# Kernel optimization log

Hardware: AMD Instinct MI355X
Metric: run time of the kernel (lower is better)

## Reference

```python
import jax, jax.numpy as jnp
import numpy as np

N_EXPERTS = 64
TOP_K = 2
LOAD_BALANCE_COEF = 0.01
D_MODEL = 4096
N_TOKENS = 16384


def setup_inputs() -> dict:
    key = jax.random.key(0)
    kx, kw = jax.random.split(key)
    x = jax.random.normal(kx, (N_TOKENS, D_MODEL), dtype=jnp.float32)
    # nn.init.normal_(gate.weight, std=0.01); shape (n_experts, d_model)
    gate_w = 0.01 * jax.random.normal(kw, (N_EXPERTS, D_MODEL), dtype=jnp.float32)
    return {"x": x, "gate_w": gate_w}


def reference(x, gate_w):
    # logits: (N, n_experts)
    logits = jnp.einsum('nd,ed->ne', x, gate_w)
    router_probs = jax.nn.softmax(logits, axis=-1)
    top_k_weights, top_k_indices = jax.lax.top_k(router_probs, TOP_K)
    routing_weights = top_k_weights / jnp.sum(top_k_weights, axis=-1, keepdims=True)
    top1 = top_k_indices[:, 0]
    one_hot = jax.nn.one_hot(top1, N_EXPERTS, dtype=x.dtype)  # (N, n_experts)
    f_i = jnp.mean(one_hot, axis=0)          # fraction of tokens per expert (detached)
    p_i = jnp.mean(router_probs, axis=0)     # mean router prob per expert (diff.)
    load_balance_loss = LOAD_BALANCE_COEF * jnp.sum(jax.lax.stop_gradient(f_i) * p_i)
    return routing_weights, top_k_indices, load_balance_loss
```

## Files before the change

kernel.cpp:

```cpp
#include <hip/hip_runtime.h>
#include <math.h>

#define N_TOKENS 16384
#define D_MODEL  4096
#define N_EXP    64

#define BK   16
#define LD   68
#define KW   (D_MODEL / 4)
#define NT   (KW / BK)
#define NBLK (N_TOKENS / 64)

__global__ void __launch_bounds__(256)
router_fused(const float* __restrict__ x, const float* __restrict__ w,
             float* __restrict__ out, float* __restrict__ block_sums) {
    __shared__ float smem[4 * 4 * BK * LD + 2 * 4 * N_EXP];

    const int tid  = threadIdx.x;
    const int wv   = tid >> 6;
    const int lane = tid & 63;
    const int tok0 = blockIdx.x * 64;

    float* xs  = smem + wv * (4 * BK * LD);
    float* wsb = xs + 2 * BK * LD;

    const int srow = lane >> 2;
    const int skc  = (lane & 3) * 4;

    const int tg   = lane & 7;
    const int eg   = lane >> 3;
    const int trow = tg * 8;
    const int ecol = eg * 8;

    const float* xp = x + (size_t)(tok0 + srow) * D_MODEL + (size_t)wv * KW + skc;
    const float* wp = w + (size_t)srow * D_MODEL + (size_t)wv * KW + skc;

    float acc[8][8] = {};

#define LOADR(q, roff) (*(const float4*)((q) + (size_t)(roff) * D_MODEL))
#define STORE_TILE(buf, v, roff) do {                      \
        (buf)[(skc + 0) * LD + srow + (roff)] = (v).x;     \
        (buf)[(skc + 1) * LD + srow + (roff)] = (v).y;     \
        (buf)[(skc + 2) * LD + srow + (roff)] = (v).z;     \
        (buf)[(skc + 3) * LD + srow + (roff)] = (v).w;     \
    } while (0)

    {
        float4 a0 = LOADR(xp, 0),  a1 = LOADR(xp, 16);
        float4 a2 = LOADR(xp, 32), a3 = LOADR(xp, 48);
        float4 b0 = LOADR(wp, 0),  b1 = LOADR(wp, 16);
        float4 b2 = LOADR(wp, 32), b3 = LOADR(wp, 48);
        STORE_TILE(xs, a0, 0);  STORE_TILE(xs, a1, 16);
        STORE_TILE(xs, a2, 32); STORE_TILE(xs, a3, 48);
        STORE_TILE(wsb, b0, 0);  STORE_TILE(wsb, b1, 16);
        STORE_TILE(wsb, b2, 32); STORE_TILE(wsb, b3, 48);
    }

    auto compute_tile = [&](const float* xb, const float* wb) {
#pragma unroll
        for (int k = 0; k < BK; ++k) {
            const float* xr = xb + k * LD + trow;
            const float* wr = wb + k * LD + ecol;
            float4 xa = *(const float4*)xr;
            float4 xc = *(const float4*)(xr + 4);
            float4 wa = *(const float4*)wr;
            float4 wc = *(const float4*)(wr + 4);
            float xf[8] = {xa.x, xa.y, xa.z, xa.w, xc.x, xc.y, xc.z, xc.w};
            float wf[8] = {wa.x, wa.y, wa.z, wa.w, wc.x, wc.y, wc.z, wc.w};
#pragma unroll
            for (int i = 0; i < 8; ++i)
#pragma unroll
                for (int j = 0; j < 8; ++j)
                    acc[i][j] = fmaf(xf[i], wf[j], acc[i][j]);
        }
    };

#pragma unroll 2
    for (int t = 0; t < NT - 1; ++t) {
        float* xb = xs  + (t & 1) * (BK * LD);
        float* wb = wsb + (t & 1) * (BK * LD);
        float* xn = xs  + ((t + 1) & 1) * (BK * LD);
        float* wn = wsb + ((t + 1) & 1) * (BK * LD);

        const float* xq = xp + (t + 1) * BK;
        const float* wq = wp + (t + 1) * BK;
        float4 a0 = LOADR(xq, 0),  a1 = LOADR(xq, 16);
        float4 a2 = LOADR(xq, 32), a3 = LOADR(xq, 48);
        float4 b0 = LOADR(wq, 0),  b1 = LOADR(wq, 16);
        float4 b2 = LOADR(wq, 32), b3 = LOADR(wq, 48);

        compute_tile(xb, wb);

        STORE_TILE(xn, a0, 0);  STORE_TILE(xn, a1, 16);
        STORE_TILE(xn, a2, 32); STORE_TILE(xn, a3, 48);
        STORE_TILE(wn, b0, 0);  STORE_TILE(wn, b1, 16);
        STORE_TILE(wn, b2, 32); STORE_TILE(wn, b3, 48);
    }
    compute_tile(xs + ((NT - 1) & 1) * (BK * LD), wsb + ((NT - 1) & 1) * (BK * LD));

    __syncthreads();

    float* tile = smem + wv * 4096;
#pragma unroll
    for (int i = 0; i < 8; ++i) {
        *(float4*)&tile[(trow + i) * 64 + ecol] =
            make_float4(acc[i][0], acc[i][1], acc[i][2], acc[i][3]);
        *(float4*)&tile[(trow + i) * 64 + ecol + 4] =
            make_float4(acc[i][4], acc[i][5], acc[i][6], acc[i][7]);
    }
    __syncthreads();

    float p_acc = 0.f, f_acc = 0.f;
#pragma unroll 1
    for (int it = 0; it < 16; ++it) {
        const int tl = wv * 16 + it;
        const int o  = tl * 64 + lane;
        float logit = smem[o] + smem[4096 + o] + smem[8192 + o] + smem[12288 + o];

        float m = logit;
#pragma unroll
        for (int off = 32; off; off >>= 1)
            m = fmaxf(m, __shfl_xor(m, off, 64));
        unsigned long long b1 = __ballot(logit == m);
        int i1 = __ffsll(b1) - 1;

        float p = expf(logit - m);
        float denom = p;
#pragma unroll
        for (int off = 32; off; off >>= 1)
            denom += __shfl_xor(denom, off, 64);

        p_acc += p / denom;
        if (lane == i1) f_acc += 1.f;

        float lx = (lane == i1) ? -__builtin_inff() : logit;
        float m2 = lx;
#pragma unroll
        for (int off = 32; off; off >>= 1)
            m2 = fmaxf(m2, __shfl_xor(m2, off, 64));
        unsigned long long b2 = __ballot(lx == m2);
        int i2 = __ffsll(b2) - 1;

        if (lane == 0) {
            float p1 = 1.0f / denom;
            float p2 = expf(m2 - m) / denom;
            float s12 = p1 + p2;
            int token = tok0 + tl;
            ((float2*)out)[token] = make_float2(p1 / s12, p2 / s12);
            ((float2*)(out + 2 * N_TOKENS))[token] =
                make_float2((float)i1, (float)i2);
        }
    }

    float* pf = smem + 4 * 4 * BK * LD;
    pf[wv * 64 + lane]       = p_acc;
    pf[256 + wv * 64 + lane] = f_acc;
    __syncthreads();
    if (tid < N_EXP) {
        float ps = pf[tid] + pf[64 + tid] + pf[128 + tid] + pf[192 + tid];
        float fs = pf[256 + tid] + pf[320 + tid] + pf[384 + tid] + pf[448 + tid];
        block_sums[(size_t)blockIdx.x * 128 + tid]      = ps;
        block_sums[(size_t)blockIdx.x * 128 + 64 + tid] = fs;
    }
}

__global__ void __launch_bounds__(256)
router_final(const float* __restrict__ block_sums, float* __restrict__ out) {
    __shared__ float sp[4][N_EXP];
    __shared__ float sf[4][N_EXP];

    int tid  = threadIdx.x;
    int wv   = tid >> 6;
    int lane = tid & 63;

    float ps = 0.f, fs = 0.f;
#pragma unroll 8
    for (int b = wv * (NBLK / 4); b < (wv + 1) * (NBLK / 4); ++b) {
        ps += block_sums[(size_t)b * 128 + lane];
        fs += block_sums[(size_t)b * 128 + 64 + lane];
    }
    sp[wv][lane] = ps;
    sf[wv][lane] = fs;
    __syncthreads();

    if (tid < N_EXP) {
        float pt = sp[0][tid] + sp[1][tid] + sp[2][tid] + sp[3][tid];
        float ft = sf[0][tid] + sf[1][tid] + sf[2][tid] + sf[3][tid];
        float v = pt * ft;
#pragma unroll
        for (int off = 1; off < 64; off <<= 1)
            v += __shfl_xor(v, off, 64);
        if (tid == 0)
            out[4 * N_TOKENS] = 0.01f * v / ((float)N_TOKENS * (float)N_TOKENS);
    }
}

extern "C" void kernel_launch(void* const* d_in, const int* in_sizes, int n_in,
                              void* d_out, int out_size, void* d_ws, size_t ws_size,
                              hipStream_t stream) {
    (void)in_sizes; (void)n_in; (void)out_size; (void)ws_size;
    const float* x = (const float*)d_in[0];
    const float* w = (const float*)d_in[1];
    float* out = (float*)d_out;
    float* block_sums = (float*)d_ws;

    router_fused<<<NBLK, 256, 0, stream>>>(x, w, out, block_sums);
    router_final<<<1, 256, 0, stream>>>(block_sums, out);
}
```

Baseline: 420.1 us.

## Repack gate weights into expert-major fragments and stream x with uniform loads

Adds a pre-kernel that transposes gate_w into a per-lane fragment layout, so each lane owns one expert and reads its weights as contiguous float4s. The main kernel drops the LDS-tiled 64x64 GEMM. Each block now handles 16 tokens, and four waves split the K dimension. x addresses are wave-uniform, which can allow scalar or broadcast loads, and partial sums are reduced in LDS. This is meant to remove the LDS staging and transpose overhead, but every block now re-reads the full weight matrix from cache and an extra launch is added.

```diff
diff --git a/kernel.cpp b/kernel.cpp
--- a/kernel.cpp
+++ b/kernel.cpp
@@ -1,121 +1,99 @@
 #include <hip/hip_runtime.h>
 #include <math.h>
+#include <stdint.h>
 
 #define N_TOKENS 16384
 #define D_MODEL  4096
 #define N_EXP    64
 
-#define BK   16
-#define LD   68
-#define KW   (D_MODEL / 4)
-#define NT   (KW / BK)
-#define NBLK (N_TOKENS / 64)
+#define T_PER 16
+#define NKS   4
+#define KSL   (D_MODEL / NKS)
+#define NG    (KSL / 8)
+#define NBLK  (N_TOKENS / T_PER)
 
 __global__ void __launch_bounds__(256)
-router_fused(const float* __restrict__ x, const float* __restrict__ w,
+w_to_frags(const float* __restrict__ w, float* __restrict__ wfr) {
+    __shared__ float t[64][65];
+    const int k0 = blockIdx.x * 64;
+    const int kc = (threadIdx.x & 15) * 4;
+    const int e0 = threadIdx.x >> 4;
+#pragma unroll
+    for (int p = 0; p < 4; ++p) {
+        int e = p * 16 + e0;
+        float4 v = *(const float4*)(w + (size_t)e * D_MODEL + k0 + kc);
+        t[kc + 0][e] = v.x; t[kc + 1][e] = v.y;
+        t[kc + 2][e] = v.z; t[kc + 3][e] = v.w;
+    }
+    __syncthreads();
+    const int e = threadIdx.x & 63;
+    const int q = threadIdx.x >> 6;
+#pragma unroll
+    for (int i = 0; i < 4; ++i) {
+        int k4l = q * 4 + i;
+        float4 v = make_float4(t[k4l * 4 + 0][e], t[k4l * 4 + 1][e],
+                               t[k4l * 4 + 2][e], t[k4l * 4 + 3][e]);
+        *(float4*)(wfr + ((size_t)(k0 / 4 + k4l) * 64 + e) * 4) = v;
+    }
+}
+
+__global__ void __launch_bounds__(256)
+router_fused(const float* __restrict__ x, const float* __restrict__ wfr,
              float* __restrict__ out, float* __restrict__ block_sums) {
-    __shared__ float smem[4 * 4 * BK * LD + 2 * 4 * N_EXP];
+    __shared__ float part[NKS * T_PER * N_EXP];
+    __shared__ float pf[2 * NKS * N_EXP];
 
     const int tid  = threadIdx.x;
     const int wv   = tid >> 6;
     const int lane = tid & 63;
-    const int tok0 = blockIdx.x * 64;
+    const int tok0 = blockIdx.x * T_PER;
 
-    float* xs  = smem + wv * (4 * BK * LD);
-    float* wsb = xs + 2 * BK * LD;
+    const int ksu = __builtin_amdgcn_readfirstlane(wv);
+    const float* xbase = x + (size_t)tok0 * D_MODEL + (size_t)ksu * KSL;
+    const float* wbase = wfr + ((size_t)ksu * (KSL / 4) * 64 + lane) * 4;
 
-    const int srow = lane >> 2;
-    const int skc  = (lane & 3) * 4;
+    float acc[T_PER] = {};
 
-    const int tg   = lane & 7;
-    const int eg   = lane >> 3;
-    const int trow = tg * 8;
-    const int ecol = eg * 8;
+    float4 w0 = *(const float4*)(wbase);
+    float4 w1 = *(const float4*)(wbase + 256);
 
-    const float* xp = x + (size_t)(tok0 + srow) * D_MODEL + (size_t)wv * KW + skc;
-    const float* wp = w + (size_t)srow * D_MODEL + (size_t)wv * KW + skc;
-
-    float acc[8][8] = {};
-
-#define LOADR(q, roff) (*(const float4*)((q) + (size_t)(roff) * D_MODEL))
-#define STORE_TILE(buf, v, roff) do {                      \
-        (buf)[(skc + 0) * LD + srow + (roff)] = (v).x;     \
-        (buf)[(skc + 1) * LD + srow + (roff)] = (v).y;     \
-        (buf)[(skc + 2) * LD + srow + (roff)] = (v).z;     \
-        (buf)[(skc + 3) * LD + srow + (roff)] = (v).w;     \
-    } while (0)
-
-    {
-        float4 a0 = LOADR(xp, 0),  a1 = LOADR(xp, 16);
-        float4 a2 = LOADR(xp, 32), a3 = LOADR(xp, 48);
-        float4 b0 = LOADR(wp, 0),  b1 = LOADR(wp, 16);
-        float4 b2 = LOADR(wp, 32), b3 = LOADR(wp, 48);
-        STORE_TILE(xs, a0, 0);  STORE_TILE(xs, a1, 16);
-        STORE_TILE(xs, a2, 32); STORE_TILE(xs, a3, 48);
-        STORE_TILE(wsb, b0, 0);  STORE_TILE(wsb, b1, 16);
-        STORE_TILE(wsb, b2, 32); STORE_TILE(wsb, b3, 48);
+    for (int g = 0; g < NG; ++g) {
+        float4 c0 = w0, c1 = w1;
+        if (g + 1 < NG) {
+            const float* nw = wbase + (size_t)(g + 1) * 512;
+            w0 = *(const float4*)(nw);
+            w1 = *(const float4*)(nw + 256);
+        }
+        const float* xg = xbase + g * 8;
+#pragma unroll
+        for (int t = 0; t < T_PER; ++t) {
+            const float* xr = xg + (size_t)t * D_MODEL;
+            float a = acc[t];
+            a = fmaf(xr[0], c0.x, a);
+            a = fmaf(xr[1], c0.y, a);
+            a = fmaf(xr[2], c0.z, a);
+            a = fmaf(xr[3], c0.w, a);
+            a = fmaf(xr[4], c1.x, a);
+            a = fmaf(xr[5], c1.y, a);
+            a = fmaf(xr[6], c1.z, a);
+            a = fmaf(xr[7], c1.w, a);
+            acc[t] = a;
+        }
     }
 
-    auto compute_tile = [&](const float* xb, const float* wb) {
 #pragma unroll
-        for (int k = 0; k < BK; ++k) {
-            const float* xr = xb + k * LD + trow;
-            const float* wr = wb + k * LD + ecol;
-            float4 xa = *(const float4*)xr;
-            float4 xc = *(const float4*)(xr + 4);
-            float4 wa = *(const float4*)wr;
-            float4 wc = *(const float4*)(wr + 4);
-            float xf[8] = {xa.x, xa.y, xa.z, xa.w, xc.x, xc.y, xc.z, xc.w};
-            float wf[8] = {wa.x, wa.y, wa.z, wa.w, wc.x, wc.y, wc.z, wc.w};
-#pragma unroll
-            for (int i = 0; i < 8; ++i)
-#pragma unroll
-                for (int j = 0; j < 8; ++j)
-                    acc[i][j] = fmaf(xf[i], wf[j], acc[i][j]);
-        }
-    };
-
-#pragma unroll 2
-    for (int t = 0; t < NT - 1; ++t) {
-        float* xb = xs  + (t & 1) * (BK * LD);
-        float* wb = wsb + (t & 1) * (BK * LD);
-        float* xn = xs  + ((t + 1) & 1) * (BK * LD);
-        float* wn = wsb + ((t + 1) & 1) * (BK * LD);
-
-        const float* xq = xp + (t + 1) * BK;
-        const float* wq = wp + (t + 1) * BK;
-        float4 a0 = LOADR(xq, 0),  a1 = LOADR(xq, 16);
-        float4 a2 = LOADR(xq, 32), a3 = LOADR(xq, 48);
-        float4 b0 = LOADR(wq, 0),  b1 = LOADR(wq, 16);
-        float4 b2 = LOADR(wq, 32), b3 = LOADR(wq, 48);
-
-        compute_tile(xb, wb);
-
-        STORE_TILE(xn, a0, 0);  STORE_TILE(xn, a1, 16);
-        STORE_TILE(xn, a2, 32); STORE_TILE(xn, a3, 48);
-        STORE_TILE(wn, b0, 0);  STORE_TILE(wn, b1, 16);
-        STORE_TILE(wn, b2, 32); STORE_TILE(wn, b3, 48);
-    }
-    compute_tile(xs + ((NT - 1) & 1) * (BK * LD), wsb + ((NT - 1) & 1) * (BK * LD));
-
-    __syncthreads();
-
-    float* tile = smem + wv * 4096;
-#pragma unroll
-    for (int i = 0; i < 8; ++i) {
-        *(float4*)&tile[(trow + i) * 64 + ecol] =
-            make_float4(acc[i][0], acc[i][1], acc[i][2], acc[i][3]);
-        *(float4*)&tile[(trow + i) * 64 + ecol + 4] =
-            make_float4(acc[i][4], acc[i][5], acc[i][6], acc[i][7]);
-    }
+    for (int t = 0; t < T_PER; ++t)
+        part[(wv * T_PER + t) * N_EXP + lane] = acc[t];
     __syncthreads();
 
     float p_acc = 0.f, f_acc = 0.f;
 #pragma unroll 1
-    for (int it = 0; it < 16; ++it) {
-        const int tl = wv * 16 + it;
-        const int o  = tl * 64 + lane;
-        float logit = smem[o] + smem[4096 + o] + smem[8192 + o] + smem[12288 + o];
+    for (int it = 0; it < 4; ++it) {
+        const int tl = it * 4 + wv;
+        float logit = part[(0 * T_PER + tl) * N_EXP + lane]
+                    + part[(1 * T_PER + tl) * N_EXP + lane]
+                    + part[(2 * T_PER + tl) * N_EXP + lane]
+                    + part[(3 * T_PER + tl) * N_EXP + lane];
 
         float m = logit;
 #pragma unroll
@@ -152,7 +130,6 @@
         }
     }
 
-    float* pf = smem + 4 * 4 * BK * LD;
     pf[wv * 64 + lane]       = p_acc;
     pf[256 + wv * 64 + lane] = f_acc;
     __syncthreads();
@@ -202,8 +179,11 @@
     const float* x = (const float*)d_in[0];
     const float* w = (const float*)d_in[1];
     float* out = (float*)d_out;
-    float* block_sums = (float*)d_ws;
 
-    router_fused<<<NBLK, 256, 0, stream>>>(x, w, out, block_sums);
+    float* wF = (float*)d_ws;
+    float* block_sums = wF + (size_t)D_MODEL * N_EXP;
+
+    w_to_frags<<<D_MODEL / 64, 256, 0, stream>>>(w, wF);
+    router_fused<<<NBLK, 256, 0, stream>>>(x, wF, out, block_sums);
     router_final<<<1, 256, 0, stream>>>(block_sums, out);
 }
```

Measured after the change: 821.2 us. 1.95x slower.
